# Kernel optimization log

Hardware: AMD Instinct MI355X
Metric: run time of the kernel (lower is better)

Reference implementation:

```python
import jax, jax.numpy as jnp
import numpy as np
from jax import lax

T, H, I, E = 1024, 1024, 512, 16          # tokens, hidden, moe_intermediate, n_routed_experts
TOP_K, N_GROUP, TOPK_GROUP = 4, 4, 2
N_SHARED = 2
I_SHARED = I * N_SHARED                    # shared-expert intermediate size
ROUTED_SCALE = 2.5


def setup_inputs() -> dict:
    key = jax.random.key(0)
    ks = jax.random.split(key, 9)
    s = lambda k, shape, fan: jax.random.normal(k, shape, jnp.float32) * (fan ** -0.5)
    return {
        "hidden_states": jax.random.normal(ks[0], (T, H), jnp.float32),
        "router_w": s(ks[1], (H, E), H),                 # gate: ReplicatedLinear(H, E)
        "e_bias": jax.random.normal(ks[2], (E,), jnp.float32) * 0.01,  # e_score_correction_bias
        "w_gate": s(ks[3], (E, H, I), H),                # routed experts gate_proj
        "w_up": s(ks[4], (E, H, I), H),                  # routed experts up_proj
        "w_down": s(ks[5], (E, I, H), I),                # routed experts down_proj
        "sw_gate": s(ks[6], (H, I_SHARED), H),           # shared experts gate_proj
        "sw_up": s(ks[7], (H, I_SHARED), H),             # shared experts up_proj
        "sw_down": s(ks[8], (I_SHARED, H), I_SHARED),    # shared experts down_proj
    }


def _grouped_topk_sigmoid(logits, e_bias):
    # DeepSeek-V3 'noaux_tc' grouped top-k with sigmoid scoring.
    scores = jax.nn.sigmoid(logits)                      # [T, E]
    sc = scores + e_bias                                 # biased scores for selection only
    g = sc.reshape(-1, N_GROUP, E // N_GROUP)
    group_scores = lax.top_k(g, 2)[0].sum(-1)            # [T, n_group]: sum of top-2 per group
    _, gidx = lax.top_k(group_scores, TOPK_GROUP)        # [T, topk_group]
    gmask = jax.nn.one_hot(gidx, N_GROUP, dtype=sc.dtype).sum(1)  # [T, n_group]
    emask = jnp.repeat(gmask, E // N_GROUP, axis=1)      # [T, E]
    masked = jnp.where(emask > 0, sc, 0.0)               # sigmoid scores are >=0
    _, tidx = lax.top_k(masked, TOP_K)                   # [T, top_k]
    w = jnp.take_along_axis(scores, tidx, axis=1)        # weights use UNbiased scores
    w = w / (w.sum(-1, keepdims=True) + 1e-20)           # norm_topk_prob=True
    # dense combine weights [T, E]
    combine = (jax.nn.one_hot(tidx, E, dtype=w.dtype) * w[..., None]).sum(1)
    return combine


def reference(hidden_states, router_w, e_bias, w_gate, w_up, w_down,
              sw_gate, sw_up, sw_down):
    x = hidden_states                                    # [T, H]
    logits = x @ router_w                                # [T, E]
    combine = _grouped_topk_sigmoid(logits, e_bias)      # [T, E]

    # routed experts: SiLU-gated MLP per expert, dense-over-experts reference
    gp = jnp.einsum('th,ehi->tei', x, w_gate)            # [T, E, I]
    up = jnp.einsum('th,ehi->tei', x, w_up)
    h = jax.nn.silu(gp) * up
    oe = jnp.einsum('tei,eih->teh', h, w_down)           # [T, E, H]
    routed = jnp.einsum('teh,te->th', oe, combine)       # [T, H]

    # shared experts MLP (reduce_results=False path), fp32 path scales routed only
    shared = (jax.nn.silu(x @ sw_gate) * (x @ sw_up)) @ sw_down  # [T, H]
    return routed * ROUTED_SCALE + shared
```

## Files before the change

### kernel.cpp

```cpp
#include <hip/hip_runtime.h>
#include <stdint.h>

#define T_TOK 1024
#define HDIM  1024
#define IDIM  512
#define NEXP  16
#define ISH   1024
#define MAXT128  48
#define HSLOTS   6144

typedef _Float16 f16;
typedef __attribute__((ext_vector_type(8))) _Float16 f16x8;
typedef __attribute__((ext_vector_type(4))) _Float16 f16x4;
typedef __attribute__((ext_vector_type(4))) float    f32x4;

__device__ __forceinline__ void gld16(const void* g, void* l) {
  __builtin_amdgcn_global_load_lds(
      (__attribute__((address_space(1))) void*)(uintptr_t)g,
      (__attribute__((address_space(3))) void*)(uint32_t)(uintptr_t)l,
      16, 0, 0);
}

__device__ __forceinline__ f16x8 ldsfrag(const f16* buf, int row, int lch) {
  int phys = lch ^ (row & 7);
  return *(const f16x8*)(buf + row * 64 + phys * 8);
}

__global__ __launch_bounds__(256) void transpose_all(
    const float* __restrict__ wg, const float* __restrict__ wu, const float* __restrict__ wd,
    const float* __restrict__ sg, const float* __restrict__ su, const float* __restrict__ sd,
    f16* __restrict__ wgT, f16* __restrict__ wuT, f16* __restrict__ wdT,
    f16* __restrict__ sgT, f16* __restrict__ suT, f16* __restrict__ sdT) {
  __shared__ float tile[64][65];
  int t = threadIdx.x;
#pragma unroll
  for (int it = 0; it < 4; it++) {
    int ti = blockIdx.x * 4 + it;
    const float* src; f16* dst; int R, C, within, clog;
    if (ti < 2048)      { int e2 = ti >> 7; within = ti & 127; R = HDIM; C = IDIM; clog = 3;
                          src = wg + (size_t)e2 * HDIM * IDIM; dst = wgT + (size_t)e2 * HDIM * IDIM; }
    else if (ti < 4096) { int u = ti - 2048; int e2 = u >> 7; within = u & 127; R = HDIM; C = IDIM; clog = 3;
                          src = wu + (size_t)e2 * HDIM * IDIM; dst = wuT + (size_t)e2 * HDIM * IDIM; }
    else if (ti < 6144) { int u = ti - 4096; int e2 = u >> 7; within = u & 127; R = IDIM; C = HDIM; clog = 4;
                          src = wd + (size_t)e2 * IDIM * HDIM; dst = wdT + (size_t)e2 * IDIM * HDIM; }
    else                { int u = ti - 6144; int which = u >> 8; within = u & 255; R = HDIM; C = ISH; clog = 4;
                          src = which == 0 ? sg : (which == 1 ? su : sd);
                          dst = which == 0 ? sgT : (which == 1 ? suT : sdT); }
    int r0 = (within >> clog) * 64, c0 = (within & ((1 << clog) - 1)) * 64;

    if (it) __syncthreads();
    int lr = t >> 4, c4 = (t & 15) * 4;
#pragma unroll
    for (int pass = 0; pass < 4; pass++) {
      int r = pass * 16 + lr;
      float4 v = *(const float4*)(src + (size_t)(r0 + r) * C + (c0 + c4));
      tile[r][c4 + 0] = v.x; tile[r][c4 + 1] = v.y;
      tile[r][c4 + 2] = v.z; tile[r][c4 + 3] = v.w;
    }
    __syncthreads();
    int oc = t >> 2, or0 = (t & 3) * 16;
    f16x8 v0, v1;
#pragma unroll
    for (int i = 0; i < 8; i++) {
      v0[i] = (f16)tile[or0 + i][oc];
      v1[i] = (f16)tile[or0 + 8 + i][oc];
    }
    f16* dp = dst + (size_t)(c0 + oc) * R + r0 + or0;
    *(f16x8*)dp = v0;
    *(f16x8*)(dp + 8) = v1;
  }
}

__global__ __launch_bounds__(256) void router_kernel(
    const float* __restrict__ x, const float* __restrict__ rw, const float* __restrict__ ebias,
    f16* __restrict__ xh, int* __restrict__ topk_i, float* __restrict__ topk_w) {
  int wave = threadIdx.x >> 6, l = threadIdx.x & 63;
  int t = blockIdx.x * 4 + wave;
  float acc[16];
#pragma unroll
  for (int e = 0; e < 16; e++) acc[e] = 0.f;
#pragma unroll
  for (int i = 0; i < 4; i++) {
    int k = i * 256 + l * 4;
    float4 xv = *(const float4*)(x + (size_t)t * HDIM + k);
    f16x4 h = { (f16)xv.x, (f16)xv.y, (f16)xv.z, (f16)xv.w };
    *(f16x4*)(xh + (size_t)t * HDIM + k) = h;
    const float* xp = &xv.x;
#pragma unroll
    for (int j = 0; j < 4; j++) {
      float xj = xp[j];
      const float4* w4 = (const float4*)(rw + (size_t)(k + j) * 16);
#pragma unroll
      for (int q = 0; q < 4; q++) {
        float4 w = w4[q];
        acc[q*4+0] += xj * w.x; acc[q*4+1] += xj * w.y;
        acc[q*4+2] += xj * w.z; acc[q*4+3] += xj * w.w;
      }
    }
  }
#pragma unroll
  for (int off = 32; off >= 1; off >>= 1)
#pragma unroll
    for (int e = 0; e < 16; e++) acc[e] += __shfl_xor(acc[e], off, 64);

  if (l == 0) {
    float s[16], sc[16];
#pragma unroll
    for (int e = 0; e < 16; e++) {
      s[e] = 1.f / (1.f + __expf(-acc[e]));
      sc[e] = s[e] + ebias[e];
    }
    float gs[4];
#pragma unroll
    for (int g = 0; g < 4; g++) {
      float a = -1e30f, b = -1e30f;
#pragma unroll
      for (int j = 0; j < 4; j++) {
        float v = sc[g*4 + j];
        if (v > a) { b = a; a = v; } else if (v > b) { b = v; }
      }
      gs[g] = a + b;
    }
    int g1 = 0;
    for (int g = 1; g < 4; g++) if (gs[g] > gs[g1]) g1 = g;
    int g2 = -1;
    for (int g = 0; g < 4; g++) if (g != g1 && (g2 < 0 || gs[g] > gs[g2])) g2 = g;
    float masked[16];
#pragma unroll
    for (int e = 0; e < 16; e++) {
      int g = e >> 2;
      masked[e] = (g == g1 || g == g2) ? sc[e] : 0.0f;
    }
    int idx[4]; float wv[4]; float denom = 1e-20f;
#pragma unroll
    for (int j = 0; j < 4; j++) {
      int best = 0; float bv = masked[0];
      for (int e = 1; e < 16; e++) if (masked[e] > bv) { bv = masked[e]; best = e; }
      idx[j] = best; wv[j] = s[best]; denom += s[best];
      masked[best] = -1e30f;
    }
#pragma unroll
    for (int j = 0; j < 4; j++) {
      topk_i[t * 4 + j] = idx[j];
      topk_w[t * 4 + j] = wv[j] / denom * 2.5f;
    }
  }
}

__global__ __launch_bounds__(1024) void scatter_kernel(
    const int* __restrict__ tki,
    int* __restrict__ tok, int* __restrict__ slotmap,
    int* __restrict__ tile_e, int* __restrict__ tile_srow,
    int* __restrict__ tile_hb, int* __restrict__ ntl) {
  __shared__ int lcnt[NEXP], lpos[NEXP], lbase[NEXP];
  int t = threadIdx.x;
  if (t < NEXP) { lcnt[t] = 0; lpos[t] = 0; }
  __syncthreads();
  int idx[4];
#pragma unroll
  for (int j = 0; j < 4; j++) idx[j] = tki[t*4+j];
#pragma unroll
  for (int j = 0; j < 4; j++) atomicAdd(&lcnt[idx[j]], 1);
  __syncthreads();
  if (t == 0) {
    int total = 0, slots = 0;
    for (int e = 0; e < NEXP; e++) {
      int c = lcnt[e], nt = (c + 127) >> 7;
      lbase[e] = slots;
      for (int j = 0; j < nt; j++) {
        tile_e[total] = e; tile_srow[total] = j * 128; tile_hb[total] = slots + j * 128; total++;
      }
      slots += nt * 128;
    }
    ntl[0] = total;
  }
  __syncthreads();
#pragma unroll
  for (int j = 0; j < 4; j++) {
    int slot = atomicAdd(&lpos[idx[j]], 1);
    tok[idx[j] * T_TOK + slot] = t;
    slotmap[t * 4 + j] = lbase[idx[j]] + slot;
  }
  __syncthreads();
  int e = t >> 6, s = t & 63;
  int c = lcnt[e];
  int top = ((c + 127) >> 7) << 7;
  for (int s2 = c + s; s2 < top; s2 += 64) tok[e * T_TOK + s2] = 0;
}

__device__ __forceinline__ f32x4 mfma16(f16x8 a, f16x8 b, f32x4 c) {
  return __builtin_amdgcn_mfma_f32_16x16x32_f16(a, b, c, 0, 0, 0);
}

__global__ __launch_bounds__(256) void gu_all(
    const f16* __restrict__ xh,
    const f16* __restrict__ sgT, const f16* __restrict__ suT, f16* __restrict__ hsh,
    const f16* __restrict__ wgT, const f16* __restrict__ wuT, f16* __restrict__ hbuf,
    const int* __restrict__ tile_e, const int* __restrict__ tile_srow,
    const int* __restrict__ tile_hb, const int* __restrict__ ntl,
    const int* __restrict__ tok) {
  int b = blockIdx.x;
  const f16 *Bg, *Bu; f16* Hdst;
  int e = 0, srow = 0, mbase, n0, N;
  bool gather = (b >= 128);
  if (!gather) {
    Bg = sgT; Bu = suT; Hdst = hsh; N = ISH;
    mbase = (b >> 4) * 128; n0 = (b & 15) * 64;
  } else {
    int rb = b - 128, by = rb >> 3;
    if (by >= ntl[0]) return;
    e = tile_e[by]; srow = tile_srow[by]; mbase = tile_hb[by];
    size_t bo = (size_t)e * IDIM * HDIM;
    Bg = wgT + bo; Bu = wuT + bo; Hdst = hbuf; N = IDIM;
    n0 = (rb & 7) * 64;
  }
  const int K = HDIM;

  __shared__ f16 As[128 * 64], Bgs[64 * 64], Bus[64 * 64];

  int tid = threadIdx.x, lane = tid & 63, wave = tid >> 6;
  int quad = lane >> 4, l15 = lane & 15;
  int r = lane >> 3, p = lane & 7;

  const f16* gb[8]; f16* lb[8];
#pragma unroll
  for (int jj = 0; jj < 8; jj++) {
    int j = wave * 8 + jj;
    int kcol = (p ^ r) << 3;
    if (j < 16) {
      int row = j * 8 + r;
      int grow = gather ? tok[e * T_TOK + srow + row] : (mbase + row);
      gb[jj] = xh + (size_t)grow * K + kcol;       lb[jj] = (f16*)As + (j << 9);
    } else if (j < 24) {
      int i = j - 16, row = i * 8 + r;
      gb[jj] = Bg + (size_t)(n0 + row) * K + kcol; lb[jj] = (f16*)Bgs + (i << 9);
    } else {
      int i = j - 24, row = i * 8 + r;
      gb[jj] = Bu + (size_t)(n0 + row) * K + kcol; lb[jj] = (f16*)Bus + (i << 9);
    }
  }

  int wr = wave >> 1, wc = wave & 1;
  f32x4 zero = {0.f, 0.f, 0.f, 0.f};
  f32x4 aG[4][2], aU[4][2];
#pragma unroll
  for (int mi = 0; mi < 4; mi++)
#pragma unroll
    for (int ni = 0; ni < 2; ni++) { aG[mi][ni] = zero; aU[mi][ni] = zero; }

  for (int kt = 0; kt < K; kt += 64) {
    __syncthreads();
#pragma unroll
    for (int jj = 0; jj < 8; jj++) gld16(gb[jj] + kt, lb[jj]);
    __syncthreads();
#pragma unroll
    for (int ks = 0; ks < 2; ks++) {
      int lch = (ks << 2) + quad;
      f16x8 a[4], g[2], u[2];
#pragma unroll
      for (int mi = 0; mi < 4; mi++) a[mi] = ldsfrag(As, 64 * wr + 16 * mi + l15, lch);
#pragma unroll
      for (int ni = 0; ni < 2; ni++) {
        g[ni] = ldsfrag(Bgs, 32 * wc + 16 * ni + l15, lch);
        u[ni] = ldsfrag(Bus, 32 * wc + 16 * ni + l15, lch);
      }
#pragma unroll
      for (int mi = 0; mi < 4; mi++)
#pragma unroll
        for (int ni = 0; ni < 2; ni++) {
          aG[mi][ni] = mfma16(a[mi], g[ni], aG[mi][ni]);
          aU[mi][ni] = mfma16(a[mi], u[ni], aU[mi][ni]);
        }
    }
  }
#pragma unroll
  for (int mi = 0; mi < 4; mi++)
#pragma unroll
    for (int ni = 0; ni < 2; ni++)
#pragma unroll
      for (int rg = 0; rg < 4; rg++) {
        int m = 64 * wr + 16 * mi + (quad << 2) + rg;
        int n = n0 + 32 * wc + 16 * ni + l15;
        float g = aG[mi][ni][rg], u = aU[mi][ni][rg];
        float val = (g / (1.f + __expf(-g))) * u;
        Hdst[(size_t)(mbase + m) * N + n] = (f16)val;
      }
}

__global__ __launch_bounds__(256) void down_all(
    const f16* __restrict__ hsh, const f16* __restrict__ sdT,
    const f16* __restrict__ hbuf, const f16* __restrict__ wdT,
    float* __restrict__ out, f16* __restrict__ odown,
    const int* __restrict__ tile_hb, const int* __restrict__ tile_e,
    const int* __restrict__ ntl) {
  int b = blockIdx.x;
  bool routed = (b >= 64);
  const f16 *A, *B; int K, abase, n0;
  if (!routed) {
    A = hsh; B = sdT; K = ISH;
    abase = (b >> 3) * 128; n0 = (b & 7) * 128;
  } else {
    int rb = b - 64, by = rb >> 3;
    if (by >= ntl[0]) return;
    abase = tile_hb[by];
    A = hbuf; B = wdT + (size_t)tile_e[by] * HDIM * IDIM; K = IDIM;
    n0 = (rb & 7) * 128;
  }

  __shared__ f16 As[128 * 64], Bs[128 * 64];

  int tid = threadIdx.x, lane = tid & 63, wave = tid >> 6;
  int quad = lane >> 4, l15 = lane & 15;
  int r = lane >> 3, p = lane & 7;

  const f16* gb[8]; f16* lb[8];
#pragma unroll
  for (int jj = 0; jj < 8; jj++) {
    int j = wave * 8 + jj;
    int kcol = (p ^ r) << 3;
    if (j < 16) {
      int row = j * 8 + r;
      gb[jj] = A + (size_t)(abase + row) * K + kcol; lb[jj] = (f16*)As + (j << 9);
    } else {
      int i = j - 16, row = i * 8 + r;
      gb[jj] = B + (size_t)(n0 + row) * K + kcol;    lb[jj] = (f16*)Bs + (i << 9);
    }
  }

  int wr = wave >> 1, wc = wave & 1;
  f32x4 zero = {0.f, 0.f, 0.f, 0.f};
  f32x4 ac[4][4];
#pragma unroll
  for (int mi = 0; mi < 4; mi++)
#pragma unroll
    for (int ni = 0; ni < 4; ni++) ac[mi][ni] = zero;

  for (int kt = 0; kt < K; kt += 64) {
    __syncthreads();
#pragma unroll
    for (int jj = 0; jj < 8; jj++) gld16(gb[jj] + kt, lb[jj]);
    __syncthreads();
#pragma unroll
    for (int ks = 0; ks < 2; ks++) {
      int lch = (ks << 2) + quad;
      f16x8 a[4], bb[4];
#pragma unroll
      for (int mi = 0; mi < 4; mi++) a[mi] = ldsfrag(As, 64 * wr + 16 * mi + l15, lch);
#pragma unroll
      for (int ni = 0; ni < 4; ni++) bb[ni] = ldsfrag(Bs, 64 * wc + 16 * ni + l15, lch);
#pragma unroll
      for (int mi = 0; mi < 4; mi++)
#pragma unroll
        for (int ni = 0; ni < 4; ni++)
          ac[mi][ni] = mfma16(a[mi], bb[ni], ac[mi][ni]);
    }
  }
#pragma unroll
  for (int mi = 0; mi < 4; mi++)
#pragma unroll
    for (int ni = 0; ni < 4; ni++)
#pragma unroll
      for (int rg = 0; rg < 4; rg++) {
        int m = 64 * wr + 16 * mi + (quad << 2) + rg;
        int n = n0 + 64 * wc + 16 * ni + l15;
        if (routed) odown[(size_t)(abase + m) * HDIM + n] = (f16)ac[mi][ni][rg];
        else        out  [(size_t)(abase + m) * HDIM + n] = ac[mi][ni][rg];
      }
}

__global__ __launch_bounds__(256) void combine_kernel(
    const f16* __restrict__ odown, const int* __restrict__ slotmap,
    const float* __restrict__ tkw, float* __restrict__ out) {
  int t = blockIdx.x;
  __shared__ int ss[4]; __shared__ float sw[4];
  if (threadIdx.x < 4) {
    ss[threadIdx.x] = slotmap[t * 4 + threadIdx.x];
    sw[threadIdx.x] = tkw[t * 4 + threadIdx.x];
  }
  __syncthreads();
  int h = threadIdx.x * 4;
  float4 acc = *(const float4*)(out + (size_t)t * HDIM + h);
#pragma unroll
  for (int j = 0; j < 4; j++) {
    f16x4 v = *(const f16x4*)(odown + (size_t)ss[j] * HDIM + h);
    float wj = sw[j];
    acc.x += wj * (float)v[0]; acc.y += wj * (float)v[1];
    acc.z += wj * (float)v[2]; acc.w += wj * (float)v[3];
  }
  *(float4*)(out + (size_t)t * HDIM + h) = acc;
}

extern "C" void kernel_launch(void* const* d_in, const int* in_sizes, int n_in,
                              void* d_out, int out_size, void* d_ws, size_t ws_size,
                              hipStream_t stream) {
  const float* x  = (const float*)d_in[0];
  const float* rw = (const float*)d_in[1];
  const float* eb = (const float*)d_in[2];
  const float* wg = (const float*)d_in[3];
  const float* wu = (const float*)d_in[4];
  const float* wd = (const float*)d_in[5];
  const float* sg = (const float*)d_in[6];
  const float* su = (const float*)d_in[7];
  const float* sd = (const float*)d_in[8];
  float* out = (float*)d_out;
  (void)in_sizes; (void)n_in; (void)out_size; (void)ws_size;

  char* w = (char*)d_ws;
  size_t off = 0;
  auto alloc = [&](size_t b) { void* p = w + off; off = (off + b + 255) & ~(size_t)255; return p; };

  f16* xh   = (f16*)alloc((size_t)T_TOK * HDIM * 2);
  f16* wgT  = (f16*)alloc((size_t)NEXP * IDIM * HDIM * 2);
  f16* wuT  = (f16*)alloc((size_t)NEXP * IDIM * HDIM * 2);
  f16* wdT  = (f16*)alloc((size_t)NEXP * HDIM * IDIM * 2);
  f16* sgT  = (f16*)alloc((size_t)ISH * HDIM * 2);
  f16* suT  = (f16*)alloc((size_t)ISH * HDIM * 2);
  f16* sdT  = (f16*)alloc((size_t)HDIM * ISH * 2);
  f16* hbuf = (f16*)alloc((size_t)HSLOTS * IDIM * 2);
  f16* hsh  = (f16*)alloc((size_t)T_TOK * ISH * 2);
  int* topk_i = (int*)alloc((size_t)T_TOK * 4 * 4);
  float* topk_w = (float*)alloc((size_t)T_TOK * 4 * 4);
  int* tok  = (int*)alloc((size_t)NEXP * T_TOK * 4);
  int* slotmap = (int*)alloc((size_t)T_TOK * 4 * 4);
  int* tile_e    = (int*)alloc(MAXT128 * 4);
  int* tile_srow = (int*)alloc(MAXT128 * 4);
  int* tile_hb   = (int*)alloc(MAXT128 * 4);
  int* ntl       = (int*)alloc(16);
  f16* odown = (f16*)wgT;

  transpose_all<<<1728, 256, 0, stream>>>(wg, wu, wd, sg, su, sd,
                                          wgT, wuT, wdT, sgT, suT, sdT);
  router_kernel<<<T_TOK / 4, 256, 0, stream>>>(x, rw, eb, xh, topk_i, topk_w);
  scatter_kernel<<<1, 1024, 0, stream>>>(topk_i, tok, slotmap,
                                         tile_e, tile_srow, tile_hb, ntl);
  gu_all<<<128 + MAXT128 * 8, 256, 0, stream>>>(
      xh, sgT, suT, hsh, wgT, wuT, hbuf, tile_e, tile_srow, tile_hb, ntl, tok);
  down_all<<<64 + MAXT128 * 8, 256, 0, stream>>>(
      hsh, sdT, hbuf, wdT, out, odown, tile_hb, tile_e, ntl);
  combine_kernel<<<T_TOK, 256, 0, stream>>>(odown, slotmap, topk_w, out);
}
```

Measured before the change: 230.0 us.

## Fuse weight transpose and router into one launch with 128x128 fp16 tiles

Merges the weight transpose/convert kernel and the router kernel into a single launch. Router blocks run after the transpose blocks in the same grid, which removes one launch and its serialization gap. The transpose now uses 128x128 tiles staged in LDS as fp16, and each thread packs pairs of columns into 16-byte stores, replacing the old loop of four 64x64 fp32 tiles per block. The change relies on the LDS padding of 130 to avoid bank conflicts and makes the combined kernel use more shared memory.

Result: no change. 229.1 us (-0.4%).

```diff
diff --git a/kernel.cpp b/kernel.cpp
--- a/kernel.cpp
+++ b/kernel.cpp
@@ -8,10 +8,12 @@
 #define ISH   1024
 #define MAXT128  48
 #define HSLOTS   6144
+#define NTTILES  1728
 
 typedef _Float16 f16;
 typedef __attribute__((ext_vector_type(8))) _Float16 f16x8;
 typedef __attribute__((ext_vector_type(4))) _Float16 f16x4;
+typedef __attribute__((ext_vector_type(2))) _Float16 f16x2;
 typedef __attribute__((ext_vector_type(4))) float    f32x4;
 
 __device__ __forceinline__ void gld16(const void* g, void* l) {
@@ -26,56 +28,75 @@
   return *(const f16x8*)(buf + row * 64 + phys * 8);
 }
 
-__global__ __launch_bounds__(256) void transpose_all(
+__global__ __launch_bounds__(256) void prep_all(
     const float* __restrict__ wg, const float* __restrict__ wu, const float* __restrict__ wd,
     const float* __restrict__ sg, const float* __restrict__ su, const float* __restrict__ sd,
     f16* __restrict__ wgT, f16* __restrict__ wuT, f16* __restrict__ wdT,
-    f16* __restrict__ sgT, f16* __restrict__ suT, f16* __restrict__ sdT) {
-  __shared__ float tile[64][65];
-  int t = threadIdx.x;
-#pragma unroll
-  for (int it = 0; it < 4; it++) {
-    int ti = blockIdx.x * 4 + it;
-    const float* src; f16* dst; int R, C, within, clog;
-    if (ti < 2048)      { int e2 = ti >> 7; within = ti & 127; R = HDIM; C = IDIM; clog = 3;
-                          src = wg + (size_t)e2 * HDIM * IDIM; dst = wgT + (size_t)e2 * HDIM * IDIM; }
-    else if (ti < 4096) { int u = ti - 2048; int e2 = u >> 7; within = u & 127; R = HDIM; C = IDIM; clog = 3;
-                          src = wu + (size_t)e2 * HDIM * IDIM; dst = wuT + (size_t)e2 * HDIM * IDIM; }
-    else if (ti < 6144) { int u = ti - 4096; int e2 = u >> 7; within = u & 127; R = IDIM; C = HDIM; clog = 4;
-                          src = wd + (size_t)e2 * IDIM * HDIM; dst = wdT + (size_t)e2 * IDIM * HDIM; }
-    else                { int u = ti - 6144; int which = u >> 8; within = u & 255; R = HDIM; C = ISH; clog = 4;
-                          src = which == 0 ? sg : (which == 1 ? su : sd);
-                          dst = which == 0 ? sgT : (which == 1 ? suT : sdT); }
-    int r0 = (within >> clog) * 64, c0 = (within & ((1 << clog) - 1)) * 64;
-
-    if (it) __syncthreads();
-    int lr = t >> 4, c4 = (t & 15) * 4;
-#pragma unroll
-    for (int pass = 0; pass < 4; pass++) {
-      int r = pass * 16 + lr;
-      float4 v = *(const float4*)(src + (size_t)(r0 + r) * C + (c0 + c4));
-      tile[r][c4 + 0] = v.x; tile[r][c4 + 1] = v.y;
-      tile[r][c4 + 2] = v.z; tile[r][c4 + 3] = v.w;
-    }
-    __syncthreads();
-    int oc = t >> 2, or0 = (t & 3) * 16;
-    f16x8 v0, v1;
-#pragma unroll
-    for (int i = 0; i < 8; i++) {
-      v0[i] = (f16)tile[or0 + i][oc];
-      v1[i] = (f16)tile[or0 + 8 + i][oc];
-    }
-    f16* dp = dst + (size_t)(c0 + oc) * R + r0 + or0;
-    *(f16x8*)dp = v0;
-    *(f16x8*)(dp + 8) = v1;
-  }
-}
-
-__global__ __launch_bounds__(256) void router_kernel(
+    f16* __restrict__ sgT, f16* __restrict__ suT, f16* __restrict__ sdT,
     const float* __restrict__ x, const float* __restrict__ rw, const float* __restrict__ ebias,
     f16* __restrict__ xh, int* __restrict__ topk_i, float* __restrict__ topk_w) {
+  int b = blockIdx.x;
+  if (b < NTTILES) {
+    const float* src; f16* dst; int R, C, rt, ct;
+    if (b < 1024) {
+      int mat = b >> 5, wi = b & 31;
+      const float* s0 = (mat < 16) ? wg : wu;
+      f16* d0 = (mat < 16) ? wgT : wuT;
+      int e = mat & 15;
+      src = s0 + (size_t)e * HDIM * IDIM; dst = d0 + (size_t)e * HDIM * IDIM;
+      R = HDIM; C = IDIM; rt = wi >> 2; ct = wi & 3;
+    } else if (b < 1536) {
+      int u = b - 1024; int e = u >> 5, wi = u & 31;
+      src = wd + (size_t)e * IDIM * HDIM; dst = wdT + (size_t)e * IDIM * HDIM;
+      R = IDIM; C = HDIM; rt = wi >> 3; ct = wi & 7;
+    } else {
+      int u = b - 1536; int which = u >> 6, wi = u & 63;
+      src = which == 0 ? sg : (which == 1 ? su : sd);
+      dst = which == 0 ? sgT : (which == 1 ? suT : sdT);
+      R = HDIM; C = ISH; rt = wi >> 3; ct = wi & 7;
+    }
+    int r0 = rt * 128, c0 = ct * 128;
+
+    __shared__ f16 tl[128 * 130];
+    int t = threadIdx.x;
+    int rr = t >> 5, c4 = (t & 31) * 4;
+#pragma unroll
+    for (int p = 0; p < 16; p++) {
+      int r = p * 8 + rr;
+      float4 v = *(const float4*)(src + (size_t)(r0 + r) * C + (c0 + c4));
+      f16x2 a = { (f16)v.x, (f16)v.y };
+      f16x2 b2 = { (f16)v.z, (f16)v.w };
+      *(f16x2*)(tl + r * 130 + c4)     = a;
+      *(f16x2*)(tl + r * 130 + c4 + 2) = b2;
+    }
+    __syncthreads();
+    int i = t & 15, cb = t >> 4;
+    int rr0 = i * 8;
+#pragma unroll
+    for (int u = 0; u < 4; u++) {
+      int cp = cb + 16 * u;
+      unsigned wv[8];
+#pragma unroll
+      for (int k = 0; k < 8; k++)
+        wv[k] = *(const unsigned*)(tl + (rr0 + k) * 130 + 2 * cp);
+      uint4 lo, hi;
+      lo.x = (wv[0] & 0xffffu) | (wv[1] << 16);
+      lo.y = (wv[2] & 0xffffu) | (wv[3] << 16);
+      lo.z = (wv[4] & 0xffffu) | (wv[5] << 16);
+      lo.w = (wv[6] & 0xffffu) | (wv[7] << 16);
+      hi.x = (wv[0] >> 16) | (wv[1] & 0xffff0000u);
+      hi.y = (wv[2] >> 16) | (wv[3] & 0xffff0000u);
+      hi.z = (wv[4] >> 16) | (wv[5] & 0xffff0000u);
+      hi.w = (wv[6] >> 16) | (wv[7] & 0xffff0000u);
+      int c = 2 * cp;
+      *(uint4*)(dst + (size_t)(c0 + c)     * R + r0 + rr0) = lo;
+      *(uint4*)(dst + (size_t)(c0 + c + 1) * R + r0 + rr0) = hi;
+    }
+    return;
+  }
+
   int wave = threadIdx.x >> 6, l = threadIdx.x & 63;
-  int t = blockIdx.x * 4 + wave;
+  int t = (b - NTTILES) * 4 + wave;
   float acc[16];
 #pragma unroll
   for (int e = 0; e < 16; e++) acc[e] = 0.f;
@@ -113,13 +134,13 @@
     float gs[4];
 #pragma unroll
     for (int g = 0; g < 4; g++) {
-      float a = -1e30f, b = -1e30f;
+      float a = -1e30f, b2 = -1e30f;
 #pragma unroll
       for (int j = 0; j < 4; j++) {
         float v = sc[g*4 + j];
-        if (v > a) { b = a; a = v; } else if (v > b) { b = v; }
-      }
-      gs[g] = a + b;
+        if (v > a) { b2 = a; a = v; } else if (v > b2) { b2 = v; }
+      }
+      gs[g] = a + b2;
     }
     int g1 = 0;
     for (int g = 1; g < 4; g++) if (gs[g] > gs[g1]) g1 = g;
@@ -428,9 +449,9 @@
   int* ntl       = (int*)alloc(16);
   f16* odown = (f16*)wgT;
 
-  transpose_all<<<1728, 256, 0, stream>>>(wg, wu, wd, sg, su, sd,
-                                          wgT, wuT, wdT, sgT, suT, sdT);
-  router_kernel<<<T_TOK / 4, 256, 0, stream>>>(x, rw, eb, xh, topk_i, topk_w);
+  prep_all<<<NTTILES + T_TOK / 4, 256, 0, stream>>>(
+      wg, wu, wd, sg, su, sd, wgT, wuT, wdT, sgT, suT, sdT,
+      x, rw, eb, xh, topk_i, topk_w);
   scatter_kernel<<<1, 1024, 0, stream>>>(topk_i, tok, slotmap,
                                          tile_e, tile_srow, tile_hb, ntl);
   gu_all<<<128 + MAXT128 * 8, 256, 0, stream>>>(
```

## Fuse weight fp32-to-fp16 conversion into GEMM B-tile staging, drop transpose kernel

Applied to the files above, without the earlier changes.

Removes the separate transpose_all pass that converted and transposed every expert and shared weight to fp16 in workspace. The gate/up and down GEMMs now read fp32 weights directly, convert them in registers and write transposed, swizzled fp16 B-tiles into padded LDS. This avoids writing and re-reading the full fp16 weight copy. In exchange, B loads become synchronous register loads of fp32 data (twice the bytes) rather than async global-to-LDS loads, and weights for experts shared by several tiles are converted repeatedly.

Measured after the change: 228.0 us. About the same (-0.9%).

```diff
diff --git a/kernel.cpp b/kernel.cpp
--- a/kernel.cpp
+++ b/kernel.cpp
@@ -21,54 +21,32 @@
       16, 0, 0);
 }
 
-__device__ __forceinline__ f16x8 ldsfrag(const f16* buf, int row, int lch) {
+__device__ __forceinline__ f16x8 ldsfragA(const f16* buf, int row, int lch) {
   int phys = lch ^ (row & 7);
   return *(const f16x8*)(buf + row * 64 + phys * 8);
 }
 
-__global__ __launch_bounds__(256) void transpose_all(
-    const float* __restrict__ wg, const float* __restrict__ wu, const float* __restrict__ wd,
-    const float* __restrict__ sg, const float* __restrict__ su, const float* __restrict__ sd,
-    f16* __restrict__ wgT, f16* __restrict__ wuT, f16* __restrict__ wdT,
-    f16* __restrict__ sgT, f16* __restrict__ suT, f16* __restrict__ sdT) {
-  __shared__ float tile[64][65];
-  int t = threadIdx.x;
-#pragma unroll
-  for (int it = 0; it < 4; it++) {
-    int ti = blockIdx.x * 4 + it;
-    const float* src; f16* dst; int R, C, within, clog;
-    if (ti < 2048)      { int e2 = ti >> 7; within = ti & 127; R = HDIM; C = IDIM; clog = 3;
-                          src = wg + (size_t)e2 * HDIM * IDIM; dst = wgT + (size_t)e2 * HDIM * IDIM; }
-    else if (ti < 4096) { int u = ti - 2048; int e2 = u >> 7; within = u & 127; R = HDIM; C = IDIM; clog = 3;
-                          src = wu + (size_t)e2 * HDIM * IDIM; dst = wuT + (size_t)e2 * HDIM * IDIM; }
-    else if (ti < 6144) { int u = ti - 4096; int e2 = u >> 7; within = u & 127; R = IDIM; C = HDIM; clog = 4;
-                          src = wd + (size_t)e2 * IDIM * HDIM; dst = wdT + (size_t)e2 * IDIM * HDIM; }
-    else                { int u = ti - 6144; int which = u >> 8; within = u & 255; R = HDIM; C = ISH; clog = 4;
-                          src = which == 0 ? sg : (which == 1 ? su : sd);
-                          dst = which == 0 ? sgT : (which == 1 ? suT : sdT); }
-    int r0 = (within >> clog) * 64, c0 = (within & ((1 << clog) - 1)) * 64;
-
-    if (it) __syncthreads();
-    int lr = t >> 4, c4 = (t & 15) * 4;
-#pragma unroll
-    for (int pass = 0; pass < 4; pass++) {
-      int r = pass * 16 + lr;
-      float4 v = *(const float4*)(src + (size_t)(r0 + r) * C + (c0 + c4));
-      tile[r][c4 + 0] = v.x; tile[r][c4 + 1] = v.y;
-      tile[r][c4 + 2] = v.z; tile[r][c4 + 3] = v.w;
-    }
-    __syncthreads();
-    int oc = t >> 2, or0 = (t & 3) * 16;
-    f16x8 v0, v1;
-#pragma unroll
-    for (int i = 0; i < 8; i++) {
-      v0[i] = (f16)tile[or0 + i][oc];
-      v1[i] = (f16)tile[or0 + 8 + i][oc];
-    }
-    f16* dp = dst + (size_t)(c0 + oc) * R + r0 + or0;
-    *(f16x8*)dp = v0;
-    *(f16x8*)(dp + 8) = v1;
-  }
+__device__ __forceinline__ f16x8 ldsfragB(const f16* buf, int n, int kc) {
+  int c = kc ^ ((n >> 3) & 7);
+  return *(const f16x8*)(buf + n * 72 + c * 8);
+}
+
+__device__ __forceinline__ void stageB(const float* __restrict__ W, int ldW,
+                                       int kt, int n0, f16* __restrict__ Bs,
+                                       int nbase, int tid) {
+  int p = tid & 31, kg = tid >> 5;
+  int n = 2 * p;
+  const float* src = W + (size_t)(kt + 8 * kg) * ldW + n0 + n;
+  float2 v[8];
+#pragma unroll
+  for (int r = 0; r < 8; r++) v[r] = *(const float2*)(src + (size_t)r * ldW);
+  f16x8 c0, c1;
+#pragma unroll
+  for (int r = 0; r < 8; r++) { c0[r] = (f16)v[r].x; c1[r] = (f16)v[r].y; }
+  int nn = nbase + n;
+  int cc = kg ^ ((nn >> 3) & 7);
+  *(f16x8*)(Bs + (size_t)nn * 72 + cc * 8) = c0;
+  *(f16x8*)(Bs + (size_t)(nn + 1) * 72 + cc * 8) = c1;
 }
 
 __global__ __launch_bounds__(256) void router_kernel(
@@ -113,13 +91,13 @@
     float gs[4];
 #pragma unroll
     for (int g = 0; g < 4; g++) {
-      float a = -1e30f, b = -1e30f;
+      float a = -1e30f, b2 = -1e30f;
 #pragma unroll
       for (int j = 0; j < 4; j++) {
         float v = sc[g*4 + j];
-        if (v > a) { b = a; a = v; } else if (v > b) { b = v; }
-      }
-      gs[g] = a + b;
+        if (v > a) { b2 = a; a = v; } else if (v > b2) { b2 = v; }
+      }
+      gs[g] = a + b2;
     }
     int g1 = 0;
     for (int g = 1; g < 4; g++) if (gs[g] > gs[g1]) g1 = g;
@@ -194,50 +172,44 @@
 
 __global__ __launch_bounds__(256) void gu_all(
     const f16* __restrict__ xh,
-    const f16* __restrict__ sgT, const f16* __restrict__ suT, f16* __restrict__ hsh,
-    const f16* __restrict__ wgT, const f16* __restrict__ wuT, f16* __restrict__ hbuf,
+    const float* __restrict__ sg, const float* __restrict__ su, f16* __restrict__ hsh,
+    const float* __restrict__ wg, const float* __restrict__ wu, f16* __restrict__ hbuf,
     const int* __restrict__ tile_e, const int* __restrict__ tile_srow,
     const int* __restrict__ tile_hb, const int* __restrict__ ntl,
     const int* __restrict__ tok) {
   int b = blockIdx.x;
-  const f16 *Bg, *Bu; f16* Hdst;
+  const float *Bg, *Bu; f16* Hdst;
   int e = 0, srow = 0, mbase, n0, N;
   bool gather = (b >= 128);
   if (!gather) {
-    Bg = sgT; Bu = suT; Hdst = hsh; N = ISH;
+    Bg = sg; Bu = su; Hdst = hsh; N = ISH;
     mbase = (b >> 4) * 128; n0 = (b & 15) * 64;
   } else {
     int rb = b - 128, by = rb >> 3;
     if (by >= ntl[0]) return;
     e = tile_e[by]; srow = tile_srow[by]; mbase = tile_hb[by];
-    size_t bo = (size_t)e * IDIM * HDIM;
-    Bg = wgT + bo; Bu = wuT + bo; Hdst = hbuf; N = IDIM;
+    size_t bo = (size_t)e * HDIM * IDIM;
+    Bg = wg + bo; Bu = wu + bo; Hdst = hbuf; N = IDIM;
     n0 = (rb & 7) * 64;
   }
   const int K = HDIM;
 
-  __shared__ f16 As[128 * 64], Bgs[64 * 64], Bus[64 * 64];
+  __shared__ f16 As[128 * 64];
+  __shared__ f16 Bgs[64 * 72], Bus[64 * 72];
 
   int tid = threadIdx.x, lane = tid & 63, wave = tid >> 6;
   int quad = lane >> 4, l15 = lane & 15;
   int r = lane >> 3, p = lane & 7;
 
-  const f16* gb[8]; f16* lb[8];
-#pragma unroll
-  for (int jj = 0; jj < 8; jj++) {
-    int j = wave * 8 + jj;
+  const f16* gbA[4]; f16* lbA[4];
+#pragma unroll
+  for (int jj = 0; jj < 4; jj++) {
+    int j = wave * 4 + jj;
     int kcol = (p ^ r) << 3;
-    if (j < 16) {
-      int row = j * 8 + r;
-      int grow = gather ? tok[e * T_TOK + srow + row] : (mbase + row);
-      gb[jj] = xh + (size_t)grow * K + kcol;       lb[jj] = (f16*)As + (j << 9);
-    } else if (j < 24) {
-      int i = j - 16, row = i * 8 + r;
-      gb[jj] = Bg + (size_t)(n0 + row) * K + kcol; lb[jj] = (f16*)Bgs + (i << 9);
-    } else {
-      int i = j - 24, row = i * 8 + r;
-      gb[jj] = Bu + (size_t)(n0 + row) * K + kcol; lb[jj] = (f16*)Bus + (i << 9);
-    }
+    int row = j * 8 + r;
+    int grow = gather ? tok[e * T_TOK + srow + row] : (mbase + row);
+    gbA[jj] = xh + (size_t)grow * K + kcol;
+    lbA[jj] = (f16*)As + (j << 9);
   }
 
   int wr = wave >> 1, wc = wave & 1;
@@ -251,18 +223,20 @@
   for (int kt = 0; kt < K; kt += 64) {
     __syncthreads();
 #pragma unroll
-    for (int jj = 0; jj < 8; jj++) gld16(gb[jj] + kt, lb[jj]);
+    for (int jj = 0; jj < 4; jj++) gld16(gbA[jj] + kt, lbA[jj]);
+    stageB(Bg, N, kt, n0, Bgs, 0, tid);
+    stageB(Bu, N, kt, n0, Bus, 0, tid);
     __syncthreads();
 #pragma unroll
     for (int ks = 0; ks < 2; ks++) {
       int lch = (ks << 2) + quad;
       f16x8 a[4], g[2], u[2];
 #pragma unroll
-      for (int mi = 0; mi < 4; mi++) a[mi] = ldsfrag(As, 64 * wr + 16 * mi + l15, lch);
+      for (int mi = 0; mi < 4; mi++) a[mi] = ldsfragA(As, 64 * wr + 16 * mi + l15, lch);
 #pragma unroll
       for (int ni = 0; ni < 2; ni++) {
-        g[ni] = ldsfrag(Bgs, 32 * wc + 16 * ni + l15, lch);
-        u[ni] = ldsfrag(Bus, 32 * wc + 16 * ni + l15, lch);
+        g[ni] = ldsfragB(Bgs, 32 * wc + 16 * ni + l15, lch);
+        u[ni] = ldsfragB(Bus, 32 * wc + 16 * ni + l15, lch);
       }
 #pragma unroll
       for (int mi = 0; mi < 4; mi++)
@@ -288,43 +262,40 @@
 }
 
 __global__ __launch_bounds__(256) void down_all(
-    const f16* __restrict__ hsh, const f16* __restrict__ sdT,
-    const f16* __restrict__ hbuf, const f16* __restrict__ wdT,
+    const f16* __restrict__ hsh, const float* __restrict__ sd,
+    const f16* __restrict__ hbuf, const float* __restrict__ wd,
     float* __restrict__ out, f16* __restrict__ odown,
     const int* __restrict__ tile_hb, const int* __restrict__ tile_e,
     const int* __restrict__ ntl) {
   int b = blockIdx.x;
   bool routed = (b >= 64);
-  const f16 *A, *B; int K, abase, n0;
+  const f16* A; const float* B; int K, abase, n0;
   if (!routed) {
-    A = hsh; B = sdT; K = ISH;
+    A = hsh; B = sd; K = ISH;
     abase = (b >> 3) * 128; n0 = (b & 7) * 128;
   } else {
     int rb = b - 64, by = rb >> 3;
     if (by >= ntl[0]) return;
     abase = tile_hb[by];
-    A = hbuf; B = wdT + (size_t)tile_e[by] * HDIM * IDIM; K = IDIM;
+    A = hbuf; B = wd + (size_t)tile_e[by] * IDIM * HDIM; K = IDIM;
     n0 = (rb & 7) * 128;
   }
 
-  __shared__ f16 As[128 * 64], Bs[128 * 64];
+  __shared__ f16 As[128 * 64];
+  __shared__ f16 Bs[128 * 72];
 
   int tid = threadIdx.x, lane = tid & 63, wave = tid >> 6;
   int quad = lane >> 4, l15 = lane & 15;
   int r = lane >> 3, p = lane & 7;
 
-  const f16* gb[8]; f16* lb[8];
-#pragma unroll
-  for (int jj = 0; jj < 8; jj++) {
-    int j = wave * 8 + jj;
+  const f16* gbA[4]; f16* lbA[4];
+#pragma unroll
+  for (int jj = 0; jj < 4; jj++) {
+    int j = wave * 4 + jj;
     int kcol = (p ^ r) << 3;
-    if (j < 16) {
-      int row = j * 8 + r;
-      gb[jj] = A + (size_t)(abase + row) * K + kcol; lb[jj] = (f16*)As + (j << 9);
-    } else {
-      int i = j - 16, row = i * 8 + r;
-      gb[jj] = B + (size_t)(n0 + row) * K + kcol;    lb[jj] = (f16*)Bs + (i << 9);
-    }
+    int row = j * 8 + r;
+    gbA[jj] = A + (size_t)(abase + row) * K + kcol;
+    lbA[jj] = (f16*)As + (j << 9);
   }
 
   int wr = wave >> 1, wc = wave & 1;
@@ -338,16 +309,18 @@
   for (int kt = 0; kt < K; kt += 64) {
     __syncthreads();
 #pragma unroll
-    for (int jj = 0; jj < 8; jj++) gld16(gb[jj] + kt, lb[jj]);
+    for (int jj = 0; jj < 4; jj++) gld16(gbA[jj] + kt, lbA[jj]);
+    stageB(B, HDIM, kt, n0,      Bs, 0,  tid);
+    stageB(B, HDIM, kt, n0 + 64, Bs, 64, tid);
     __syncthreads();
 #pragma unroll
     for (int ks = 0; ks < 2; ks++) {
       int lch = (ks << 2) + quad;
       f16x8 a[4], bb[4];
 #pragma unroll
-      for (int mi = 0; mi < 4; mi++) a[mi] = ldsfrag(As, 64 * wr + 16 * mi + l15, lch);
-#pragma unroll
-      for (int ni = 0; ni < 4; ni++) bb[ni] = ldsfrag(Bs, 64 * wc + 16 * ni + l15, lch);
+      for (int mi = 0; mi < 4; mi++) a[mi] = ldsfragA(As, 64 * wr + 16 * mi + l15, lch);
+#pragma unroll
+      for (int ni = 0; ni < 4; ni++) bb[ni] = ldsfragB(Bs, 64 * wc + 16 * ni + l15, lch);
 #pragma unroll
       for (int mi = 0; mi < 4; mi++)
 #pragma unroll
@@ -410,14 +383,9 @@
   auto alloc = [&](size_t b) { void* p = w + off; off = (off + b + 255) & ~(size_t)255; return p; };
 
   f16* xh   = (f16*)alloc((size_t)T_TOK * HDIM * 2);
-  f16* wgT  = (f16*)alloc((size_t)NEXP * IDIM * HDIM * 2);
-  f16* wuT  = (f16*)alloc((size_t)NEXP * IDIM * HDIM * 2);
-  f16* wdT  = (f16*)alloc((size_t)NEXP * HDIM * IDIM * 2);
-  f16* sgT  = (f16*)alloc((size_t)ISH * HDIM * 2);
-  f16* suT  = (f16*)alloc((size_t)ISH * HDIM * 2);
-  f16* sdT  = (f16*)alloc((size_t)HDIM * ISH * 2);
   f16* hbuf = (f16*)alloc((size_t)HSLOTS * IDIM * 2);
   f16* hsh  = (f16*)alloc((size_t)T_TOK * ISH * 2);
+  f16* odown = (f16*)alloc((size_t)HSLOTS * HDIM * 2);
   int* topk_i = (int*)alloc((size_t)T_TOK * 4 * 4);
   float* topk_w = (float*)alloc((size_t)T_TOK * 4 * 4);
   int* tok  = (int*)alloc((size_t)NEXP * T_TOK * 4);
@@ -426,16 +394,13 @@
   int* tile_srow = (int*)alloc(MAXT128 * 4);
   int* tile_hb   = (int*)alloc(MAXT128 * 4);
   int* ntl       = (int*)alloc(16);
-  f16* odown = (f16*)wgT;
-
-  transpose_all<<<1728, 256, 0, stream>>>(wg, wu, wd, sg, su, sd,
-                                          wgT, wuT, wdT, sgT, suT, sdT);
+
   router_kernel<<<T_TOK / 4, 256, 0, stream>>>(x, rw, eb, xh, topk_i, topk_w);
   scatter_kernel<<<1, 1024, 0, stream>>>(topk_i, tok, slotmap,
                                          tile_e, tile_srow, tile_hb, ntl);
   gu_all<<<128 + MAXT128 * 8, 256, 0, stream>>>(
-      xh, sgT, suT, hsh, wgT, wuT, hbuf, tile_e, tile_srow, tile_hb, ntl, tok);
+      xh, sg, su, hsh, wg, wu, hbuf, tile_e, tile_srow, tile_hb, ntl, tok);
   down_all<<<64 + MAXT128 * 8, 256, 0, stream>>>(
-      hsh, sdT, hbuf, wdT, out, odown, tile_hb, tile_e, ntl);
+      hsh, sd, hbuf, wd, out, odown, tile_hb, tile_e, ntl);
   combine_kernel<<<T_TOK, 256, 0, stream>>>(odown, slotmap, topk_w, out);
 }
```
